# Kernel optimization log

Hardware: AMD Instinct MI355X
Metric: run time of the kernel (lower is better)

## Reference

```python
import jax, jax.numpy as jnp
import numpy as np

N_SENT = 131072
NUM_BAGS = 8192
REL_DIM = 690
NUM_CLASSES = 53


def setup_inputs() -> dict:
    key = jax.random.key(0)
    k1, k2, k3, k4, k5, k6 = jax.random.split(key, 6)
    x = jax.random.normal(k1, (N_SENT, REL_DIM), dtype=jnp.float32)
    relation_weight = jax.random.normal(k2, (NUM_CLASSES, REL_DIM), dtype=jnp.float32) * 0.06
    attention_weight = jax.random.normal(k3, (NUM_CLASSES, REL_DIM), dtype=jnp.float32) * 0.06
    bias = jax.random.normal(k4, (NUM_CLASSES,), dtype=jnp.float32)
    attention_query = jax.random.randint(k5, (N_SENT,), 0, NUM_CLASSES, dtype=jnp.int32)
    # strictly increasing bag boundaries: 0 < b_1 < ... < b_{B-1} < N
    interior = jax.random.choice(k6, N_SENT - 1, shape=(NUM_BAGS - 1,), replace=False) + 1
    scope = jnp.concatenate([jnp.zeros((1,), jnp.int32),
                             jnp.sort(interior).astype(jnp.int32),
                             jnp.full((1,), N_SENT, jnp.int32)])
    return {"x": x, "relation_weight": relation_weight,
            "attention_weight": attention_weight, "bias": bias,
            "attention_query": attention_query, "scope": scope}


def reference(x, relation_weight, attention_weight, bias, attention_query, scope):
    N = x.shape[0]
    B = scope.shape[0] - 1  # num bags
    # map each sentence to its bag: scope[b] <= i < scope[b+1]
    seg = jnp.searchsorted(scope[1:], jnp.arange(N), side="right")

    # per-sentence attention logit: sum(x * att_emb * rel_emb) over feature dim
    rel_q = relation_weight[attention_query]   # [N, D]
    att_q = attention_weight[attention_query]  # [N, D]
    logit = jnp.sum(x * att_q * rel_q, axis=1)  # [N]

    # segment softmax over each bag (numerically stable)
    seg_max = jax.ops.segment_max(logit, seg, num_segments=B)  # [B]
    e = jnp.exp(logit - seg_max[seg])                           # [N]
    denom = jax.ops.segment_sum(e, seg, num_segments=B)        # [B]
    w = e / denom[seg]                                          # [N]

    # attention-weighted bag representation
    bag_repre = jax.ops.segment_sum(w[:, None] * x, seg, num_segments=B)  # [B, D]

    # dropout with drop_prob = 0.0 -> identity
    logits = bag_repre @ relation_weight.T + bias  # [B, C]
    return logits
```

## Files before the change

kernel.cpp:

```cpp
#include <hip/hip_runtime.h>
#include <math.h>

#define NSENT 131072
#define NBAGS 8192
#define DIM   690
#define NCLS  53
#define PAIRS 345

__global__ void comb_kernel(const float* __restrict__ att,
                            const float* __restrict__ rel,
                            float* __restrict__ comb) {
    int i = blockIdx.x * 256 + threadIdx.x;
    if (i < NCLS * DIM) comb[i] = att[i] * rel[i];
}

template <bool USE_COMB>
__global__ __launch_bounds__(256) void bag_attn_kernel(
        const float* __restrict__ x,
        const float* __restrict__ rel,
        const float* __restrict__ att,
        const float* __restrict__ bias,
        const int*   __restrict__ query,
        const int*   __restrict__ scope,
        const float* __restrict__ comb,
        float*       __restrict__ out) {
    const int b     = blockIdx.x;
    const int tid   = threadIdx.x;
    const int wave  = tid >> 6;
    const int lane  = tid & 63;

    const int start = scope[b];
    const int end   = scope[b + 1];

    float2 acc[6];
#pragma unroll
    for (int k = 0; k < 6; ++k) acc[k] = make_float2(0.f, 0.f);
    float m = -INFINITY;
    float l = 0.f;

    for (int i = start + wave; i < end; i += 4) {
        const float2* xrow = (const float2*)(x + (size_t)i * DIM);
        const int q = query[i];

        float2 xv[6];
        float partial = 0.f;
        if (USE_COMB) {
            const float2* crow = (const float2*)(comb + (size_t)q * DIM);
#pragma unroll
            for (int k = 0; k < 6; ++k) {
                const int p = lane + 64 * k;
                if (p < PAIRS) {
                    xv[k] = xrow[p];
                    const float2 cv = crow[p];
                    partial += xv[k].x * cv.x + xv[k].y * cv.y;
                } else {
                    xv[k] = make_float2(0.f, 0.f);
                }
            }
        } else {
            const float2* rrow = (const float2*)(rel + (size_t)q * DIM);
            const float2* arow = (const float2*)(att + (size_t)q * DIM);
#pragma unroll
            for (int k = 0; k < 6; ++k) {
                const int p = lane + 64 * k;
                if (p < PAIRS) {
                    xv[k] = xrow[p];
                    const float2 rv = rrow[p];
                    const float2 av = arow[p];
                    partial += xv[k].x * rv.x * av.x + xv[k].y * rv.y * av.y;
                } else {
                    xv[k] = make_float2(0.f, 0.f);
                }
            }
        }

#pragma unroll
        for (int off = 32; off >= 1; off >>= 1)
            partial += __shfl_xor(partial, off, 64);
        const float logit = partial;

        const float mn    = fmaxf(m, logit);
        const float scale = expf(m - mn);
        const float e     = expf(logit - mn);
        l = l * scale + e;
#pragma unroll
        for (int k = 0; k < 6; ++k) {
            acc[k].x = acc[k].x * scale + e * xv[k].x;
            acc[k].y = acc[k].y * scale + e * xv[k].y;
        }
        m = mn;
    }

    __shared__ float s_m[4];
    __shared__ float s_l[4];
    __shared__ float s_acc[4][DIM];
    __shared__ float s_rep[DIM];

    if (lane == 0) { s_m[wave] = m; s_l[wave] = l; }
    __syncthreads();

    const float M = fmaxf(fmaxf(s_m[0], s_m[1]), fmaxf(s_m[2], s_m[3]));
    const float factor = (l > 0.f) ? expf(m - M) : 0.f;
#pragma unroll
    for (int k = 0; k < 6; ++k) {
        const int p = lane + 64 * k;
        if (p < PAIRS) {
            s_acc[wave][2 * p]     = acc[k].x * factor;
            s_acc[wave][2 * p + 1] = acc[k].y * factor;
        }
    }
    __syncthreads();

    float Ltot = 0.f;
#pragma unroll
    for (int w = 0; w < 4; ++w) {
        const float fw = (s_l[w] > 0.f) ? expf(s_m[w] - M) : 0.f;
        Ltot += s_l[w] * fw;
    }
    const float inv = 1.f / Ltot;

    for (int d = tid; d < DIM; d += 256) {
        s_rep[d] = (s_acc[0][d] + s_acc[1][d] + s_acc[2][d] + s_acc[3][d]) * inv;
    }
    __syncthreads();

    for (int c = wave; c < NCLS; c += 4) {
        const float2* rrow = (const float2*)(rel + (size_t)c * DIM);
        float partial = 0.f;
#pragma unroll
        for (int k = 0; k < 6; ++k) {
            const int p = lane + 64 * k;
            if (p < PAIRS) {
                const float2 rv = rrow[p];
                partial += rv.x * s_rep[2 * p] + rv.y * s_rep[2 * p + 1];
            }
        }
#pragma unroll
        for (int off = 32; off >= 1; off >>= 1)
            partial += __shfl_xor(partial, off, 64);
        if (lane == 0) out[(size_t)b * NCLS + c] = partial + bias[c];
    }
}

extern "C" void kernel_launch(void* const* d_in, const int* in_sizes, int n_in,
                              void* d_out, int out_size, void* d_ws, size_t ws_size,
                              hipStream_t stream) {
    const float* x     = (const float*)d_in[0];
    const float* rel   = (const float*)d_in[1];
    const float* att   = (const float*)d_in[2];
    const float* bias  = (const float*)d_in[3];
    const int*   query = (const int*)d_in[4];
    const int*   scope = (const int*)d_in[5];
    float*       out   = (float*)d_out;

    const size_t comb_bytes = (size_t)NCLS * DIM * sizeof(float);
    if (ws_size >= comb_bytes) {
        float* comb = (float*)d_ws;
        comb_kernel<<<(NCLS * DIM + 255) / 256, 256, 0, stream>>>(att, rel, comb);
        bag_attn_kernel<true><<<NBAGS, 256, 0, stream>>>(
            x, rel, att, bias, query, scope, comb, out);
    } else {
        bag_attn_kernel<false><<<NBAGS, 256, 0, stream>>>(
            x, rel, att, bias, query, scope, nullptr, out);
    }
}
```

Measured before the change: 597.7 us.

## Assign one wave per bag and drop cross-wave shared-memory merge

Each 64-lane wave now processes a whole bag, with four bags per block, in place of four waves splitting one bag. This removes the shared-memory merge, the block barriers and the multi-wave softmax combine. The online softmax gains a lazy rescale that only updates the running max when the new logit exceeds it by more than 8, and uses fast __expf. The final classifier dot products run from registers two classes at a time, and lanes write results coalesced. Load balance now depends on bag size per wave, and fewer waves serve long bags.

```diff
diff --git a/kernel.cpp b/kernel.cpp
--- a/kernel.cpp
+++ b/kernel.cpp
@@ -15,7 +15,7 @@
 }
 
 template <bool USE_COMB>
-__global__ __launch_bounds__(256) void bag_attn_kernel(
+__global__ __launch_bounds__(256, 8) void bag_attn_wave_kernel(
         const float* __restrict__ x,
         const float* __restrict__ rel,
         const float* __restrict__ att,
@@ -24,10 +24,10 @@
         const int*   __restrict__ scope,
         const float* __restrict__ comb,
         float*       __restrict__ out) {
-    const int b     = blockIdx.x;
-    const int tid   = threadIdx.x;
-    const int wave  = tid >> 6;
-    const int lane  = tid & 63;
+    const int tid  = threadIdx.x;
+    const int wave = tid >> 6;
+    const int lane = tid & 63;
+    const int b    = blockIdx.x * 4 + wave;
 
     const int start = scope[b];
     const int end   = scope[b + 1];
@@ -38,7 +38,7 @@
     float m = -INFINITY;
     float l = 0.f;
 
-    for (int i = start + wave; i < end; i += 4) {
+    for (int i = start; i < end; ++i) {
         const float2* xrow = (const float2*)(x + (size_t)i * DIM);
         const int q = query[i];
 
@@ -52,7 +52,8 @@
                 if (p < PAIRS) {
                     xv[k] = xrow[p];
                     const float2 cv = crow[p];
-                    partial += xv[k].x * cv.x + xv[k].y * cv.y;
+                    partial = fmaf(xv[k].x, cv.x, partial);
+                    partial = fmaf(xv[k].y, cv.y, partial);
                 } else {
                     xv[k] = make_float2(0.f, 0.f);
                 }
@@ -67,7 +68,8 @@
                     xv[k] = xrow[p];
                     const float2 rv = rrow[p];
                     const float2 av = arow[p];
-                    partial += xv[k].x * rv.x * av.x + xv[k].y * rv.y * av.y;
+                    partial = fmaf(xv[k].x, rv.x * av.x, partial);
+                    partial = fmaf(xv[k].y, rv.y * av.y, partial);
                 } else {
                     xv[k] = make_float2(0.f, 0.f);
                 }
@@ -77,69 +79,76 @@
 #pragma unroll
         for (int off = 32; off >= 1; off >>= 1)
             partial += __shfl_xor(partial, off, 64);
-        const float logit = partial;
 
-        const float mn    = fmaxf(m, logit);
-        const float scale = expf(m - mn);
-        const float e     = expf(logit - mn);
-        l = l * scale + e;
+        const float d = partial - m;
+        if (d <= 8.0f) {
+            const float e = __expf(d);
 #pragma unroll
-        for (int k = 0; k < 6; ++k) {
-            acc[k].x = acc[k].x * scale + e * xv[k].x;
-            acc[k].y = acc[k].y * scale + e * xv[k].y;
+            for (int k = 0; k < 6; ++k) {
+                acc[k].x = fmaf(e, xv[k].x, acc[k].x);
+                acc[k].y = fmaf(e, xv[k].y, acc[k].y);
+            }
+            l += e;
+        } else {
+            const float r = __expf(-d);
+#pragma unroll
+            for (int k = 0; k < 6; ++k) {
+                acc[k].x = fmaf(acc[k].x, r, xv[k].x);
+                acc[k].y = fmaf(acc[k].y, r, xv[k].y);
+            }
+            l = fmaf(l, r, 1.f);
+            m = partial;
         }
-        m = mn;
     }
 
-    __shared__ float s_m[4];
-    __shared__ float s_l[4];
-    __shared__ float s_acc[4][DIM];
-    __shared__ float s_rep[DIM];
+    const float inv = 1.f / l;
+    float res = (lane < NCLS) ? bias[lane] : 0.f;
 
-    if (lane == 0) { s_m[wave] = m; s_l[wave] = l; }
-    __syncthreads();
-
-    const float M = fmaxf(fmaxf(s_m[0], s_m[1]), fmaxf(s_m[2], s_m[3]));
-    const float factor = (l > 0.f) ? expf(m - M) : 0.f;
-#pragma unroll
-    for (int k = 0; k < 6; ++k) {
-        const int p = lane + 64 * k;
-        if (p < PAIRS) {
-            s_acc[wave][2 * p]     = acc[k].x * factor;
-            s_acc[wave][2 * p + 1] = acc[k].y * factor;
-        }
-    }
-    __syncthreads();
-
-    float Ltot = 0.f;
-#pragma unroll
-    for (int w = 0; w < 4; ++w) {
-        const float fw = (s_l[w] > 0.f) ? expf(s_m[w] - M) : 0.f;
-        Ltot += s_l[w] * fw;
-    }
-    const float inv = 1.f / Ltot;
-
-    for (int d = tid; d < DIM; d += 256) {
-        s_rep[d] = (s_acc[0][d] + s_acc[1][d] + s_acc[2][d] + s_acc[3][d]) * inv;
-    }
-    __syncthreads();
-
-    for (int c = wave; c < NCLS; c += 4) {
-        const float2* rrow = (const float2*)(rel + (size_t)c * DIM);
-        float partial = 0.f;
+#pragma unroll 1
+    for (int c = 0; c < NCLS - 1; c += 2) {
+        const float2* r0 = (const float2*)(rel + (size_t)c * DIM);
+        const float2* r1 = (const float2*)(rel + (size_t)(c + 1) * DIM);
+        float p0 = 0.f, p1 = 0.f;
 #pragma unroll
         for (int k = 0; k < 6; ++k) {
             const int p = lane + 64 * k;
             if (p < PAIRS) {
-                const float2 rv = rrow[p];
-                partial += rv.x * s_rep[2 * p] + rv.y * s_rep[2 * p + 1];
+                const float2 v0 = r0[p];
+                const float2 v1 = r1[p];
+                p0 = fmaf(v0.x, acc[k].x, p0);
+                p0 = fmaf(v0.y, acc[k].y, p0);
+                p1 = fmaf(v1.x, acc[k].x, p1);
+                p1 = fmaf(v1.y, acc[k].y, p1);
+            }
+        }
+#pragma unroll
+        for (int off = 32; off >= 1; off >>= 1) {
+            p0 += __shfl_xor(p0, off, 64);
+            p1 += __shfl_xor(p1, off, 64);
+        }
+        if (lane == c)     res = fmaf(p0, inv, res);
+        if (lane == c + 1) res = fmaf(p1, inv, res);
+    }
+    {
+        const int c = NCLS - 1;
+        const float2* r0 = (const float2*)(rel + (size_t)c * DIM);
+        float p0 = 0.f;
+#pragma unroll
+        for (int k = 0; k < 6; ++k) {
+            const int p = lane + 64 * k;
+            if (p < PAIRS) {
+                const float2 v0 = r0[p];
+                p0 = fmaf(v0.x, acc[k].x, p0);
+                p0 = fmaf(v0.y, acc[k].y, p0);
             }
         }
 #pragma unroll
         for (int off = 32; off >= 1; off >>= 1)
-            partial += __shfl_xor(partial, off, 64);
-        if (lane == 0) out[(size_t)b * NCLS + c] = partial + bias[c];
+            p0 += __shfl_xor(p0, off, 64);
+        if (lane == c) res = fmaf(p0, inv, res);
     }
+
+    if (lane < NCLS) out[(size_t)b * NCLS + lane] = res;
 }
 
 extern "C" void kernel_launch(void* const* d_in, const int* in_sizes, int n_in,
@@ -157,10 +166,10 @@
     if (ws_size >= comb_bytes) {
         float* comb = (float*)d_ws;
         comb_kernel<<<(NCLS * DIM + 255) / 256, 256, 0, stream>>>(att, rel, comb);
-        bag_attn_kernel<true><<<NBAGS, 256, 0, stream>>>(
+        bag_attn_wave_kernel<true><<<NBAGS / 4, 256, 0, stream>>>(
             x, rel, att, bias, query, scope, comb, out);
     } else {
-        bag_attn_kernel<false><<<NBAGS, 256, 0, stream>>>(
+        bag_attn_wave_kernel<false><<<NBAGS / 4, 256, 0, stream>>>(
             x, rel, att, bias, query, scope, nullptr, out);
     }
 }
```

New measurement: 685.1 us. 1.15x slower.
